# Kernel tuning notes

Hardware: AMD Instinct MI355X
Metric: run time of the kernel (lower is better)

## Reference

```python
import jax, jax.numpy as jnp
import numpy as np

E = 512
H = 8
D = E // H  # head_dim = 64
SCALE = D ** -0.5
NEG_INF = float('-inf')


def layer_norm(x, g, b, eps=1e-5):
    mu = jnp.mean(x, axis=-1, keepdims=True)
    var = jnp.var(x, axis=-1, keepdims=True)
    return (x - mu) * jax.lax.rsqrt(var + eps) * g + b


def setup_inputs() -> dict:
    key = jax.random.key(0)
    ks = jax.random.split(key, 16)
    B, Q, K = 4, 2048, 2048
    inp = {
        'query': jax.random.normal(ks[0], (B, Q, E), jnp.float32),
        'key_value': jax.random.normal(ks[1], (B, K, E), jnp.float32),
        'kv_mask': jax.random.randint(ks[2], (B, K), 0, 2) > 0,
        'sparse_mask': jax.random.randint(ks[3], (B, Q, K), 0, 2) > 0,
        'ln_q_g': jnp.ones((E,), jnp.float32),
        'ln_q_b': jnp.zeros((E,), jnp.float32),
        'ln_kv_g': jnp.ones((E,), jnp.float32),
        'ln_kv_b': jnp.zeros((E,), jnp.float32),
        # Linear weights stored as (in, out): y = x @ W + b
        'Wq': jax.random.normal(ks[4], (E, E), jnp.float32) * (E ** -0.5),
        'bq': jnp.zeros((E,), jnp.float32),
        'Wk': jax.random.normal(ks[5], (E, E), jnp.float32) * (E ** -0.5),
        'bk': jnp.zeros((E,), jnp.float32),
        'Wv': jax.random.normal(ks[6], (E, E), jnp.float32) * (E ** -0.5),
        'bv': jnp.zeros((E,), jnp.float32),
        'Wo': jax.random.normal(ks[7], (E, E), jnp.float32) * (E ** -0.5),
        'bo': jnp.zeros((E,), jnp.float32),
    }
    return inp


def reference(query, key_value, kv_mask, sparse_mask,
              ln_q_g, ln_q_b, ln_kv_g, ln_kv_b,
              Wq, bq, Wk, bk, Wv, bv, Wo, bo):
    B, Qn, _ = query.shape
    Kn = key_value.shape[1]
    qn = layer_norm(query, ln_q_g, ln_q_b)
    kvn = layer_norm(key_value, ln_kv_g, ln_kv_b)
    q = (qn @ Wq + bq).reshape(B, Qn, H, D)
    k = (kvn @ Wk + bk).reshape(B, Kn, H, D)
    v = (kvn @ Wv + bv).reshape(B, Kn, H, D)
    # scores: [B, H, Q, K]
    scores = jnp.einsum('bqhd,bkhd->bhqk', q, k) * SCALE
    mask = kv_mask[:, None, None, :] & sparse_mask[:, None, :, :]
    scores = jnp.where(mask, scores, NEG_INF)
    attn = jax.nn.softmax(scores, axis=-1)
    # nan_to_num(0): rows with no valid key -> all-zero weights
    valid_row = jnp.any(mask, axis=-1, keepdims=True)
    attn = jnp.where(valid_row, attn, 0.0)
    out = jnp.einsum('bhqk,bkhd->bqhd', attn, v).reshape(B, Qn, E)
    return out @ Wo + bo
```

## Files before the change

kernel.cpp:

```cpp
#include <hip/hip_runtime.h>
#include <hip/hip_bf16.h>
#include <math.h>

typedef unsigned short ushort_t;
typedef __attribute__((ext_vector_type(8))) __bf16 bf16x8;
typedef __attribute__((ext_vector_type(4))) float f32x4;
typedef __attribute__((ext_vector_type(16))) float f32x16;
typedef __attribute__((ext_vector_type(4))) unsigned int u32x4;

#define E_DIM 512
#define HEADS 8
#define HD 64
#define SEQ 2048
#define NROWS 8192
#define QSCALE 0.18033688011112042f

static __device__ __forceinline__ unsigned short f2b(float f) {
  unsigned int x;
  __builtin_memcpy(&x, &f, 4);
  x += 0x7fffu + ((x >> 16) & 1u);
  return (unsigned short)(x >> 16);
}

static __device__ __forceinline__ unsigned cvt_pk_bf16(float lo, float hi) {
  unsigned r;
  asm("v_cvt_pk_bf16_f32 %0, %1, %2" : "=v"(r) : "v"(lo), "v"(hi));
  return r;
}

static __device__ __forceinline__ float fexp2(float x) {
  float r;
  asm("v_exp_f32 %0, %1" : "=v"(r) : "v"(x));
  return r;
}

static __device__ __forceinline__ unsigned bitmask1(unsigned v, int off) {
#if __has_builtin(__builtin_amdgcn_sbfe)
  return (unsigned)__builtin_amdgcn_sbfe((int)v, off, 1);
#else
  return (unsigned)((int)(v << (31 - off)) >> 31);
#endif
}

static __device__ __forceinline__ int swz(int row, int col) {
  return row * 64 + ((((col >> 3) ^ (row & 7)) & 7) << 3) + (col & 7);
}

static __device__ __forceinline__ void gl2lds16(const ushort_t* g, ushort_t* s) {
#if __has_builtin(__builtin_amdgcn_global_load_lds)
  __builtin_amdgcn_global_load_lds(
      (const __attribute__((address_space(1))) unsigned int*)(uintptr_t)g,
      (__attribute__((address_space(3))) unsigned int*)(uintptr_t)s,
      16, 0, 0);
#else
  int l = threadIdx.x & 63;
  *(u32x4*)(s + l * 8) = *(const u32x4*)g;
#endif
}

__launch_bounds__(256)
__global__ void prep_kernel(const float* __restrict__ Wq, const float* __restrict__ Wk,
                            const float* __restrict__ Wv, const float* __restrict__ Wo,
                            ushort_t* __restrict__ WT,
                            const int* __restrict__ kvm, const int* __restrict__ sp,
                            unsigned long long* __restrict__ bits,
                            const float* __restrict__ xq, const float* __restrict__ xkv,
                            const float* __restrict__ gq, const float* __restrict__ bq,
                            const float* __restrict__ gkv, const float* __restrict__ bkv,
                            ushort_t* __restrict__ yq, ushort_t* __restrict__ ykv) {
  int blk = blockIdx.x;
  int t = threadIdx.x;
  if (blk < 1024) {
    int z = blk >> 8, rem = blk & 255;
    const float* in = (z == 0) ? Wq : (z == 1) ? Wk : (z == 2) ? Wv : Wo;
    ushort_t* o = WT + (size_t)z * E_DIM * E_DIM;
    __shared__ float tile[32 * 33];
    int tx = t & 31, ty = t >> 5;
    int n0 = (rem & 15) * 32, k0 = (rem >> 4) * 32;
#pragma unroll
    for (int i = 0; i < 4; ++i) {
      int k = ty + i * 8;
      tile[k * 33 + tx] = in[(k0 + k) * E_DIM + n0 + tx];
    }
    __syncthreads();
#pragma unroll
    for (int i = 0; i < 4; ++i) {
      int n = ty + i * 8;
      o[(n0 + n) * E_DIM + k0 + tx] = f2b(tile[tx * 33 + n]);
    }
  } else if (blk < 3072) {
    int w = t >> 6, l = t & 63;
    int row = (blk - 1024) * 4 + w;
    int b = row >> 11;
    const int* sprow = sp + ((size_t)row << 11);
    const int* kvrow = kvm + (b << 11);
    unsigned long long* out = bits + ((size_t)row << 5);
#pragma unroll 4
    for (int it = 0; it < 32; ++it) {
      int k = it * 64 + l;
      unsigned long long m = __ballot(sprow[k] != 0 && kvrow[k] != 0);
      if (l == 0) out[it] = m;
    }
  } else {
    int idx = blk - 3072;
    int which = idx >> 11;
    const float* x = which ? xkv : xq;
    const float* g = which ? gkv : gq;
    const float* bb = which ? bkv : bq;
    ushort_t* y = which ? ykv : yq;
    int w = t >> 6, l = t & 63;
    int row = (idx & 2047) * 4 + w;
    f32x4 x0 = *(const f32x4*)&x[row * E_DIM + l * 8];
    f32x4 x1 = *(const f32x4*)&x[row * E_DIM + l * 8 + 4];
    float xf[8], s = 0.f, ss = 0.f;
#pragma unroll
    for (int j = 0; j < 8; ++j) {
      xf[j] = (j < 4) ? x0[j] : x1[j - 4];
      s += xf[j];
      ss += xf[j] * xf[j];
    }
#pragma unroll
    for (int off = 32; off > 0; off >>= 1) {
      s += __shfl_xor(s, off);
      ss += __shfl_xor(ss, off);
    }
    float mu = s * (1.f / 512.f);
    float var = fmaxf(ss * (1.f / 512.f) - mu * mu, 0.f);
    float rs = rsqrtf(var + 1e-5f);
    f32x4 g0 = *(const f32x4*)&g[l * 8];
    f32x4 g1 = *(const f32x4*)&g[l * 8 + 4];
    f32x4 b0 = *(const f32x4*)&bb[l * 8];
    f32x4 b1 = *(const f32x4*)&bb[l * 8 + 4];
#pragma unroll
    for (int j = 0; j < 8; ++j) {
      float gv = (j < 4) ? g0[j] : g1[j - 4];
      float bv = (j < 4) ? b0[j] : b1[j - 4];
      y[row * E_DIM + l * 8 + j] = f2b((xf[j] - mu) * rs * gv + bv);
    }
  }
}

template <int MODE>
static __device__ __forceinline__ void gemm_core64(ushort_t* lA, ushort_t* lB,
                                                   const ushort_t* __restrict__ A,
                                                   const ushort_t* __restrict__ WT,
                                                   const float* __restrict__ bias,
                                                   void* Cv, float scale, int m0, int n0) {
  int t = threadIdx.x, w = t >> 6, l = t & 63;
  int quad = l >> 4, l15 = l & 15;
  int wm_ = w >> 1, wn_ = w & 1;
  int csrc = ((l & 7) ^ (l >> 3)) * 8;
  int rln = l >> 3;

  f32x4 acc[4][2] = {};
  for (int kk = 0; kk < E_DIM; kk += 64) {
    __syncthreads();
#pragma unroll
    for (int i = 0; i < 4; ++i) {
      int r0 = i * 32 + w * 8;
      gl2lds16(&A[(size_t)(m0 + r0 + rln) * E_DIM + kk + csrc], &lA[r0 * 64]);
    }
#pragma unroll
    for (int i = 0; i < 2; ++i) {
      int r0 = i * 32 + w * 8;
      gl2lds16(&WT[(size_t)(n0 + r0 + rln) * E_DIM + kk + csrc], &lB[r0 * 64]);
    }
    __syncthreads();
#pragma unroll
    for (int ks = 0; ks < 2; ++ks) {
      bf16x8 af[4], bf[2];
#pragma unroll
      for (int mt = 0; mt < 4; ++mt)
        af[mt] = *(const bf16x8*)&lA[swz(wm_ * 64 + mt * 16 + l15, ks * 32 + quad * 8)];
#pragma unroll
      for (int nt = 0; nt < 2; ++nt)
        bf[nt] = *(const bf16x8*)&lB[swz(wn_ * 32 + nt * 16 + l15, ks * 32 + quad * 8)];
#pragma unroll
      for (int mt = 0; mt < 4; ++mt)
#pragma unroll
        for (int nt = 0; nt < 2; ++nt)
          acc[mt][nt] = __builtin_amdgcn_mfma_f32_16x16x32_bf16(af[mt], bf[nt], acc[mt][nt], 0, 0, 0);
    }
  }

#pragma unroll
  for (int nt = 0; nt < 2; ++nt) {
    int col = n0 + wn_ * 32 + nt * 16 + l15;
    float bv = bias[col];
    if constexpr (MODE == 2) {
      int h = col >> 6, d = col & 63;
#pragma unroll
      for (int mt = 0; mt < 4; ++mt) {
        int row = m0 + wm_ * 64 + mt * 16 + quad * 4;
        int b = row >> 11, k = row & 2047;
        union { ushort_t u[4]; uint2 v; } pk;
#pragma unroll
        for (int r = 0; r < 4; ++r) pk.u[r] = f2b(acc[mt][nt][r] + bv);
        *(uint2*)&((ushort_t*)Cv)[((((size_t)(b * HEADS + h)) * HD + d) << 11) + k] = pk.v;
      }
    } else {
#pragma unroll
      for (int mt = 0; mt < 4; ++mt) {
#pragma unroll
        for (int r = 0; r < 4; ++r) {
          int rowm = m0 + wm_ * 64 + mt * 16 + quad * 4 + r;
          float val = (acc[mt][nt][r] + bv) * scale;
          if constexpr (MODE == 0)
            ((ushort_t*)Cv)[rowm * E_DIM + col] = f2b(val);
          else
            ((float*)Cv)[rowm * E_DIM + col] = val;
        }
      }
    }
  }
}

__launch_bounds__(256)
__global__ void proj3_kernel(const ushort_t* __restrict__ qn, const ushort_t* __restrict__ WTq,
                             const float* __restrict__ bq, ushort_t* __restrict__ qp,
                             const ushort_t* __restrict__ kvn, const ushort_t* __restrict__ WTv,
                             const float* __restrict__ bv, ushort_t* __restrict__ Vt,
                             const ushort_t* __restrict__ WTk, const float* __restrict__ bk,
                             ushort_t* __restrict__ kp, int zbase) {
  __shared__ ushort_t lA[128 * 64];
  __shared__ ushort_t lB[64 * 64];
  int flat = blockIdx.x;
  int chunk = gridDim.x >> 3;
  int work = (flat & 7) * chunk + (flat >> 3);
  int z = zbase + (work >> 9);
  int r = work & 511;
  int m0 = (r >> 3) * 128, n0 = (r & 7) * 64;
  if (z == 0)      gemm_core64<0>(lA, lB, qn,  WTq, bq, qp, QSCALE, m0, n0);
  else if (z == 1) gemm_core64<2>(lA, lB, kvn, WTv, bv, Vt, 1.f,    m0, n0);
  else             gemm_core64<0>(lA, lB, kvn, WTk, bk, kp, 1.f,    m0, n0);
}

__launch_bounds__(256)
__global__ void out_kernel(const ushort_t* __restrict__ A, const ushort_t* __restrict__ WT,
                           const float* __restrict__ bias, float* __restrict__ C) {
  __shared__ ushort_t lA[128 * 64];
  __shared__ ushort_t lB[64 * 64];
  int flat = blockIdx.x;
  int work = (flat & 7) * 64 + (flat >> 3);
  int m0 = (work >> 3) * 128, n0 = (work & 7) * 64;
  gemm_core64<1>(lA, lB, A, WT, bias, C, 1.f, m0, n0);
}

__launch_bounds__(256)
__global__ void attn_kernel(const ushort_t* __restrict__ Qp, const ushort_t* __restrict__ Kp,
                            const ushort_t* __restrict__ Vt,
                            const unsigned long long* __restrict__ bits,
                            ushort_t* __restrict__ ctx) {
  __shared__ __align__(16) char smemb[40960];
  ushort_t* sQ = (ushort_t*)smemb;
  int t = threadIdx.x, w = t >> 6, l = t & 63;
  int qw = w & 1, ks = w >> 1;
  ushort_t* sK = (ushort_t*)(smemb + 8192 + ks * 8192);
  ushort_t* sV = (ushort_t*)(smemb + 24576 + ks * 8192);
  int l31 = l & 31, half = l >> 5;

  int flat = blockIdx.x;
  int work = (flat & 7) * 128 + (flat >> 3);
  int qblk = work & 31;
  int h = (work >> 5) & 7;
  int b = work >> 8;
  int q0 = qblk * 64;
  int bh = b * HEADS + h;
  int myq = qw * 32 + l31;
  int csrc = ((l & 7) ^ (l >> 3)) * 8;
  int rln = l >> 3;

#pragma unroll
  for (int it = 0; it < 2; ++it) {
    int r0 = w * 16 + it * 8;
    gl2lds16(&Qp[(size_t)(b * SEQ + q0 + r0 + rln) * E_DIM + h * HD + csrc], &sQ[r0 * 64]);
  }

  const unsigned long long* mrow = bits + ((size_t)(b * SEQ + q0 + myq) << 5);
  f32x16 o0 = {}, o1 = {}, lacc = {};
  bf16x8 qf[4];
  union { unsigned u[4]; bf16x8 v; } onec;
#pragma unroll
  for (int i = 0; i < 4; ++i) onec.u[i] = 0x3f803f80u;

  for (int t16 = 0; t16 < 16; ++t16) {
    int kt = t16 * 2 + ks;
    int k0 = kt * 64;
    unsigned long long wmask = mrow[kt];
    __syncthreads();
#pragma unroll
    for (int it = 0; it < 4; ++it) {
      int r0 = (it * 2 + qw) * 8;
      gl2lds16(&Kp[(size_t)(b * SEQ + k0 + r0 + rln) * E_DIM + h * HD + csrc], &sK[r0 * 64]);
      gl2lds16(&Vt[((size_t)bh * HD + r0 + rln) * SEQ + k0 + csrc], &sV[r0 * 64]);
    }
    __syncthreads();
    if (t16 == 0) {
#pragma unroll
      for (int ds = 0; ds < 4; ++ds)
        qf[ds] = *(const bf16x8*)&sQ[swz(myq, ds * 16 + 8 * half)];
    }

    f32x16 s0 = {}, s1 = {};
    __builtin_amdgcn_s_setprio(1);
#pragma unroll
    for (int ds = 0; ds < 4; ++ds) {
      bf16x8 kf0 = *(const bf16x8*)&sK[swz(l31, ds * 16 + 8 * half)];
      bf16x8 kf1 = *(const bf16x8*)&sK[swz(32 + l31, ds * 16 + 8 * half)];
      s0 = __builtin_amdgcn_mfma_f32_32x32x16_bf16(kf0, qf[ds], s0, 0, 0, 0);
      s1 = __builtin_amdgcn_mfma_f32_32x32x16_bf16(kf1, qf[ds], s1, 0, 0, 0);
    }
    __builtin_amdgcn_s_setprio(0);

    bf16x8 pf[4];
#pragma unroll
    for (int kt2 = 0; kt2 < 2; ++kt2) {
      const f32x16& sv = kt2 ? s1 : s0;
      unsigned h32 = ((unsigned)(wmask >> (32 * kt2))) >> (4 * half);
      unsigned wa[4], wb[4];
#pragma unroll
      for (int g = 0; g < 4; ++g) {
        unsigned q0u = __float_as_uint(fexp2(sv[g * 4 + 0])) & bitmask1(h32, 8 * g + 0);
        unsigned q1u = __float_as_uint(fexp2(sv[g * 4 + 1])) & bitmask1(h32, 8 * g + 1);
        unsigned q2u = __float_as_uint(fexp2(sv[g * 4 + 2])) & bitmask1(h32, 8 * g + 2);
        unsigned q3u = __float_as_uint(fexp2(sv[g * 4 + 3])) & bitmask1(h32, 8 * g + 3);
        wa[g] = cvt_pk_bf16(__uint_as_float(q0u), __uint_as_float(q1u));
        wb[g] = cvt_pk_bf16(__uint_as_float(q2u), __uint_as_float(q3u));
      }
      asm("v_permlane32_swap_b32 %0, %1" : "+v"(wa[0]), "+v"(wa[1]));
      asm("v_permlane32_swap_b32 %0, %1" : "+v"(wb[0]), "+v"(wb[1]));
      asm("v_permlane32_swap_b32 %0, %1" : "+v"(wa[2]), "+v"(wa[3]));
      asm("v_permlane32_swap_b32 %0, %1" : "+v"(wb[2]), "+v"(wb[3]));
      union { unsigned u[4]; bf16x8 v; } f0, f1;
      f0.u[0] = wa[0]; f0.u[1] = wb[0]; f0.u[2] = wa[1]; f0.u[3] = wb[1];
      f1.u[0] = wa[2]; f1.u[1] = wb[2]; f1.u[2] = wa[3]; f1.u[3] = wb[3];
      pf[kt2 * 2 + 0] = f0.v;
      pf[kt2 * 2 + 1] = f1.v;
    }

    __builtin_amdgcn_s_setprio(1);
#pragma unroll
    for (int ksp = 0; ksp < 4; ++ksp) {
      bf16x8 vf0 = *(const bf16x8*)&sV[swz(l31, ksp * 16 + 8 * half)];
      bf16x8 vf1 = *(const bf16x8*)&sV[swz(32 + l31, ksp * 16 + 8 * half)];
      o0 = __builtin_amdgcn_mfma_f32_32x32x16_bf16(vf0, pf[ksp], o0, 0, 0, 0);
      o1 = __builtin_amdgcn_mfma_f32_32x32x16_bf16(vf1, pf[ksp], o1, 0, 0, 0);
      lacc = __builtin_amdgcn_mfma_f32_32x32x16_bf16(onec.v, pf[ksp], lacc, 0, 0, 0);
    }
    __builtin_amdgcn_s_setprio(0);
  }

  float lsum = lacc[0];

  __syncthreads();
  float* mrg = (float*)(smemb + 8192);
  if (ks == 1) {
    float* e = mrg + (qw * 64 + l) * 33;
#pragma unroll
    for (int r = 0; r < 16; ++r) e[r] = o0[r];
#pragma unroll
    for (int r = 0; r < 16; ++r) e[16 + r] = o1[r];
    e[32] = lsum;
  }
  __syncthreads();
  if (ks == 0) {
    const float* e = mrg + (qw * 64 + l) * 33;
#pragma unroll
    for (int r = 0; r < 16; ++r) o0[r] += e[r];
#pragma unroll
    for (int r = 0; r < 16; ++r) o1[r] += e[16 + r];
    lsum += e[32];
    float inv = (lsum > 0.f) ? 1.f / lsum : 0.f;
    size_t base = (size_t)(b * SEQ + q0 + myq) * E_DIM + h * HD;
#pragma unroll
    for (int dt = 0; dt < 2; ++dt) {
      const f32x16& oo = dt ? o1 : o0;
#pragma unroll
      for (int g = 0; g < 4; ++g) {
        union { ushort_t u[4]; uint2 v; } ov;
#pragma unroll
        for (int r = 0; r < 4; ++r) ov.u[r] = f2b(oo[g * 4 + r] * inv);
        *(uint2*)&ctx[base + dt * 32 + g * 8 + 4 * half] = ov.v;
      }
    }
  }
}

extern "C" void kernel_launch(void* const* d_in, const int* in_sizes, int n_in,
                              void* d_out, int out_size, void* d_ws, size_t ws_size,
                              hipStream_t stream) {
  const float* query     = (const float*)d_in[0];
  const float* key_value = (const float*)d_in[1];
  const int*   kv_mask   = (const int*)d_in[2];
  const int*   sp_mask   = (const int*)d_in[3];
  const float* ln_q_g  = (const float*)d_in[4];
  const float* ln_q_b  = (const float*)d_in[5];
  const float* ln_kv_g = (const float*)d_in[6];
  const float* ln_kv_b = (const float*)d_in[7];
  const float* Wq = (const float*)d_in[8];
  const float* bq = (const float*)d_in[9];
  const float* Wk = (const float*)d_in[10];
  const float* bk = (const float*)d_in[11];
  const float* Wv = (const float*)d_in[12];
  const float* bv = (const float*)d_in[13];
  const float* Wo = (const float*)d_in[14];
  const float* bo = (const float*)d_in[15];

  const size_t NB = (size_t)NROWS * E_DIM;
  char* ws = (char*)d_ws;
  ushort_t* bufA = (ushort_t*)ws;
  ushort_t* bufB = bufA + NB;
  ushort_t* WT   = bufB + NB;
  ushort_t* WTq = WT;
  ushort_t* WTk = WTq + E_DIM * E_DIM;
  ushort_t* WTv = WTk + E_DIM * E_DIM;
  ushort_t* WTo = WTv + E_DIM * E_DIM;
  unsigned long long* bits = (unsigned long long*)(WTo + E_DIM * E_DIM);
  ushort_t* bufC = (ushort_t*)(ws + (20u << 20));

  ushort_t* dlo = (ushort_t*)d_out;
  ushort_t* dhi = dlo + NB;

  bool fused = ws_size >= (28u << 20);
  ushort_t* kp = fused ? bufC : dlo;

  prep_kernel<<<7168, 256, 0, stream>>>(Wq, Wk, Wv, Wo, WT, kv_mask, sp_mask, bits,
                                        query, key_value, ln_q_g, ln_q_b, ln_kv_g, ln_kv_b,
                                        dlo, bufA);

  if (fused) {
    proj3_kernel<<<1536, 256, 0, stream>>>(dlo, WTq, bq, dhi,
                                           bufA, WTv, bv, bufB,
                                           WTk, bk, bufC, 0);
  } else {
    proj3_kernel<<<1024, 256, 0, stream>>>(dlo, WTq, bq, dhi,
                                           bufA, WTv, bv, bufB,
                                           WTk, bk, dlo, 0);
    proj3_kernel<<<512, 256, 0, stream>>>(dlo, WTq, bq, dhi,
                                          bufA, WTv, bv, bufB,
                                          WTk, bk, dlo, 2);
  }

  attn_kernel<<<1024, 256, 0, stream>>>(dhi, kp, bufB, bits, bufA);

  out_kernel<<<512, 256, 0, stream>>>(bufA, WTo, bo, (float*)d_out);
}
```

Before: 261.1 us.

## Split attention key range across four wave groups and vectorize mask bit packing

The attention kernel now launches 512 threads per block, so four key-split wave pairs each process a quarter of the key tiles instead of two halves, with a three-way LDS merge at the end. The shared buffer grows to 64 KB, and Q is loaded once up front instead of inside the first loop iteration. The mask-packing prep path now reads four ints per lane and uses four ballots, which changes the bit layout of the packed mask; the attention consumer's bit indexing is updated to match. This aims to add parallelism per tile and cut the cost of mask packing, at the price of higher LDS use per block, which may lower occupancy.

```diff
diff --git a/kernel.cpp b/kernel.cpp
--- a/kernel.cpp
+++ b/kernel.cpp
@@ -92,14 +92,27 @@
     int w = t >> 6, l = t & 63;
     int row = (blk - 1024) * 4 + w;
     int b = row >> 11;
-    const int* sprow = sp + ((size_t)row << 11);
-    const int* kvrow = kvm + (b << 11);
+    const int4* sprow = (const int4*)(sp + ((size_t)row << 11));
+    const int4* kvrow = (const int4*)(kvm + ((size_t)b << 11));
     unsigned long long* out = bits + ((size_t)row << 5);
-#pragma unroll 4
-    for (int it = 0; it < 32; ++it) {
-      int k = it * 64 + l;
-      unsigned long long m = __ballot(sprow[k] != 0 && kvrow[k] != 0);
-      if (l == 0) out[it] = m;
+#pragma unroll
+    for (int it = 0; it < 8; ++it) {
+      int4 s4 = sprow[it * 64 + l];
+      int4 k4 = kvrow[it * 64 + l];
+      unsigned nib = (unsigned)((s4.x && k4.x) ? 1 : 0) | ((s4.y && k4.y) ? 2u : 0)
+                   | ((s4.z && k4.z) ? 4u : 0) | ((s4.w && k4.w) ? 8u : 0);
+      unsigned long long b0 = __ballot((nib & 1u) != 0);
+      unsigned long long b1 = __ballot((nib & 2u) != 0);
+      unsigned long long b2 = __ballot((nib & 4u) != 0);
+      unsigned long long b3 = __ballot((nib & 8u) != 0);
+      if (l < 4) {
+        int m16 = l * 16;
+        unsigned long long wv = ((b0 >> m16) & 0xFFFFull)
+                              | (((b1 >> m16) & 0xFFFFull) << 16)
+                              | (((b2 >> m16) & 0xFFFFull) << 32)
+                              | (((b3 >> m16) & 0xFFFFull) << 48);
+        out[it * 4 + l] = wv;
+      }
     }
   } else {
     int idx = blk - 3072;
@@ -246,17 +259,17 @@
   gemm_core64<1>(lA, lB, A, WT, bias, C, 1.f, m0, n0);
 }
 
-__launch_bounds__(256)
+__launch_bounds__(512)
 __global__ void attn_kernel(const ushort_t* __restrict__ Qp, const ushort_t* __restrict__ Kp,
                             const ushort_t* __restrict__ Vt,
                             const unsigned long long* __restrict__ bits,
                             ushort_t* __restrict__ ctx) {
-  __shared__ __align__(16) char smemb[40960];
-  ushort_t* sQ = (ushort_t*)smemb;
+  __shared__ __align__(16) char smemb[65536];
   int t = threadIdx.x, w = t >> 6, l = t & 63;
   int qw = w & 1, ks = w >> 1;
-  ushort_t* sK = (ushort_t*)(smemb + 8192 + ks * 8192);
-  ushort_t* sV = (ushort_t*)(smemb + 24576 + ks * 8192);
+  ushort_t* sQ = (ushort_t*)smemb;
+  ushort_t* sK = (ushort_t*)(smemb + ks * 8192);
+  ushort_t* sV = (ushort_t*)(smemb + 32768 + ks * 8192);
   int l31 = l & 31, half = l >> 5;
 
   int flat = blockIdx.x;
@@ -270,21 +283,21 @@
   int csrc = ((l & 7) ^ (l >> 3)) * 8;
   int rln = l >> 3;
 
-#pragma unroll
-  for (int it = 0; it < 2; ++it) {
-    int r0 = w * 16 + it * 8;
-    gl2lds16(&Qp[(size_t)(b * SEQ + q0 + r0 + rln) * E_DIM + h * HD + csrc], &sQ[r0 * 64]);
-  }
+  gl2lds16(&Qp[(size_t)(b * SEQ + q0 + w * 8 + rln) * E_DIM + h * HD + csrc], &sQ[w * 8 * 64]);
+  __syncthreads();
+  bf16x8 qf[4];
+#pragma unroll
+  for (int ds = 0; ds < 4; ++ds)
+    qf[ds] = *(const bf16x8*)&sQ[swz(myq, ds * 16 + 8 * half)];
 
   const unsigned long long* mrow = bits + ((size_t)(b * SEQ + q0 + myq) << 5);
   f32x16 o0 = {}, o1 = {}, lacc = {};
-  bf16x8 qf[4];
   union { unsigned u[4]; bf16x8 v; } onec;
 #pragma unroll
   for (int i = 0; i < 4; ++i) onec.u[i] = 0x3f803f80u;
 
-  for (int t16 = 0; t16 < 16; ++t16) {
-    int kt = t16 * 2 + ks;
+  for (int t8 = 0; t8 < 8; ++t8) {
+    int kt = t8 * 4 + ks;
     int k0 = kt * 64;
     unsigned long long wmask = mrow[kt];
     __syncthreads();
@@ -295,11 +308,6 @@
       gl2lds16(&Vt[((size_t)bh * HD + r0 + rln) * SEQ + k0 + csrc], &sV[r0 * 64]);
     }
     __syncthreads();
-    if (t16 == 0) {
-#pragma unroll
-      for (int ds = 0; ds < 4; ++ds)
-        qf[ds] = *(const bf16x8*)&sQ[swz(myq, ds * 16 + 8 * half)];
-    }
 
     f32x16 s0 = {}, s1 = {};
     __builtin_amdgcn_s_setprio(1);
@@ -312,18 +320,19 @@
     }
     __builtin_amdgcn_s_setprio(0);
 
+    unsigned mlo = (unsigned)wmask, mhi = (unsigned)(wmask >> 32);
     bf16x8 pf[4];
 #pragma unroll
     for (int kt2 = 0; kt2 < 2; ++kt2) {
       const f32x16& sv = kt2 ? s1 : s0;
-      unsigned h32 = ((unsigned)(wmask >> (32 * kt2))) >> (4 * half);
       unsigned wa[4], wb[4];
 #pragma unroll
       for (int g = 0; g < 4; ++g) {
-        unsigned q0u = __float_as_uint(fexp2(sv[g * 4 + 0])) & bitmask1(h32, 8 * g + 0);
-        unsigned q1u = __float_as_uint(fexp2(sv[g * 4 + 1])) & bitmask1(h32, 8 * g + 1);
-        unsigned q2u = __float_as_uint(fexp2(sv[g * 4 + 2])) & bitmask1(h32, 8 * g + 2);
-        unsigned q3u = __float_as_uint(fexp2(sv[g * 4 + 3])) & bitmask1(h32, 8 * g + 3);
+        int bb = 8 * kt2 + 2 * g + half;
+        unsigned q0u = __float_as_uint(fexp2(sv[g * 4 + 0])) & bitmask1(mlo, bb);
+        unsigned q1u = __float_as_uint(fexp2(sv[g * 4 + 1])) & bitmask1(mlo, bb + 16);
+        unsigned q2u = __float_as_uint(fexp2(sv[g * 4 + 2])) & bitmask1(mhi, bb);
+        unsigned q3u = __float_as_uint(fexp2(sv[g * 4 + 3])) & bitmask1(mhi, bb + 16);
         wa[g] = cvt_pk_bf16(__uint_as_float(q0u), __uint_as_float(q1u));
         wb[g] = cvt_pk_bf16(__uint_as_float(q2u), __uint_as_float(q3u));
       }
@@ -353,9 +362,9 @@
   float lsum = lacc[0];
 
   __syncthreads();
-  float* mrg = (float*)(smemb + 8192);
-  if (ks == 1) {
-    float* e = mrg + (qw * 64 + l) * 33;
+  float* mrg = (float*)smemb;
+  if (ks != 0) {
+    float* e = mrg + (((ks - 1) * 2 + qw) * 64 + l) * 33;
 #pragma unroll
     for (int r = 0; r < 16; ++r) e[r] = o0[r];
 #pragma unroll
@@ -364,12 +373,15 @@
   }
   __syncthreads();
   if (ks == 0) {
-    const float* e = mrg + (qw * 64 + l) * 33;
-#pragma unroll
-    for (int r = 0; r < 16; ++r) o0[r] += e[r];
-#pragma unroll
-    for (int r = 0; r < 16; ++r) o1[r] += e[16 + r];
-    lsum += e[32];
+#pragma unroll
+    for (int s3 = 0; s3 < 3; ++s3) {
+      const float* e = mrg + ((s3 * 2 + qw) * 64 + l) * 33;
+#pragma unroll
+      for (int r = 0; r < 16; ++r) o0[r] += e[r];
+#pragma unroll
+      for (int r = 0; r < 16; ++r) o1[r] += e[16 + r];
+      lsum += e[32];
+    }
     float inv = (lsum > 0.f) ? 1.f / lsum : 0.f;
     size_t base = (size_t)(b * SEQ + q0 + myq) * E_DIM + h * HD;
 #pragma unroll
@@ -441,7 +453,7 @@
                                           WTk, bk, dlo, 2);
   }
 
-  attn_kernel<<<1024, 256, 0, stream>>>(dhi, kp, bufB, bits, bufA);
+  attn_kernel<<<1024, 512, 0, stream>>>(dhi, kp, bufB, bits, bufA);
 
   out_kernel<<<512, 256, 0, stream>>>(bufA, WTo, bo, (float*)d_out);
 }
```

New measurement: 261.0 us. About the same (-0.1%).
